# Performance work log

Hardware: AMD Instinct MI355X
Metric: run time of the kernel (lower is better)

## Reference

```python
import jax, jax.numpy as jnp
import numpy as np

DT = 0.01


def setup_inputs() -> dict:
    key = jax.random.key(0)
    ks = jax.random.split(key, 16)
    B, T, IN, S, N, OUT, H = 512, 2048, 32, 16, 128, 8, 64
    sc = 0.1
    return {
        "obs": jax.random.normal(ks[0], (B, T, IN), jnp.float32),
        "x0": jnp.zeros((B, S), jnp.float32),
        "A_T": sc * jax.random.normal(ks[1], (S, S), jnp.float32),
        "Bw_T": sc * jax.random.normal(ks[2], (N, S), jnp.float32),
        "By_T": sc * jax.random.normal(ks[3], (IN, S), jnp.float32),
        "Cv_T": sc * jax.random.normal(ks[4], (S, N), jnp.float32),
        "Dvy_T": sc * jax.random.normal(ks[5], (IN, N), jnp.float32),
        "Cu_T": sc * jax.random.normal(ks[6], (S, OUT), jnp.float32),
        "Duw_T": sc * jax.random.normal(ks[7], (N, OUT), jnp.float32),
        "Duy_T": sc * jax.random.normal(ks[8], (IN, OUT), jnp.float32),
        "log_stds": jnp.full((OUT,), -1.6094379124341003, jnp.float32),
        "W1": sc * jax.random.normal(ks[9], (IN, H), jnp.float32),
        "b1": jnp.zeros((H,), jnp.float32),
        "W2": sc * jax.random.normal(ks[10], (H, H), jnp.float32),
        "b2": jnp.zeros((H,), jnp.float32),
        "W3": sc * jax.random.normal(ks[11], (H, 1), jnp.float32),
        "b3": jnp.zeros((1,), jnp.float32),
    }


def reference(obs, x0, A_T, Bw_T, By_T, Cv_T, Dvy_T, Cu_T, Duw_T, Duy_T,
              log_stds, W1, b1, W2, b2, W3, b3):
    B, T, _ = obs.shape

    def xdot(x, y, w=None):
        if w is None:
            w = jnp.tanh(x @ Cv_T + y @ Dvy_T)
        return x @ A_T + w @ Bw_T + y @ By_T

    def step(x, y):
        # y: [B, IN], x: [B, S]
        w = jnp.tanh(x @ Cv_T + y @ Dvy_T)          # [B, N]
        u = x @ Cu_T + w @ Duw_T + y @ Duy_T        # [B, OUT]
        k1 = xdot(x, y, w=w)
        k2 = xdot(x + DT * k1 / 2, y)
        k3 = xdot(x + DT * k2 / 2, y)
        k4 = xdot(x + DT * k3, y)
        x_next = x + DT / 6 * (k1 + 2 * k2 + 2 * k3 + k4)
        return x_next, u

    obs_t = jnp.swapaxes(obs, 0, 1)                 # [T, B, IN]
    x_final, actions_t = jax.lax.scan(step, x0, obs_t)
    actions = jnp.swapaxes(actions_t, 0, 1)         # [B, T, OUT]

    log_stds_rep = jnp.broadcast_to(log_stds, actions.shape[:2] + log_stds.shape)
    outputs = jnp.concatenate((actions, log_stds_rep), axis=2)

    # value baseline MLP over raw observations
    h = jnp.tanh(obs @ W1 + b1)
    h = jnp.tanh(h @ W2 + b2)
    value = (h @ W3 + b3).reshape(-1)               # [B*T]
    return outputs, x_final, value
```

## Files before the change

### kernel.cpp

```cpp
#include <hip/hip_runtime.h>


#define B_SZ  512
#define T_LEN 2048
#define IN_D  32
#define S_D   16
#define N_D   128
#define OUT_D 8
#define H_D   64
#define DT_C  0.01f

typedef unsigned short u16;
typedef unsigned int   u32;
typedef unsigned int uv2 __attribute__((ext_vector_type(2)));

__device__ __forceinline__ float bf2f(u16 u){ return __uint_as_float(((u32)u)<<16); }
__device__ __forceinline__ float lo2f(u32 w){ return __uint_as_float(w<<16); }
__device__ __forceinline__ float hi2f(u32 w){ return __uint_as_float(w & 0xffff0000u); }
__device__ __forceinline__ u16 f2bf(float f){
    u32 u = __float_as_uint(f);
    u32 r = (u + 0x7fffu + ((u>>16)&1u)) >> 16;
    return (u16)r;
}
__device__ __forceinline__ float fast_tanh(float a){
    float e = __builtin_amdgcn_exp2f(a * 2.8853900817779268f);
    float r = __builtin_amdgcn_rcpf(e + 1.0f);
    return fmaf(-2.0f, r, 1.0f);
}
__device__ __forceinline__ u32 getc(const uint4& v, int c){
    return c==0 ? v.x : c==1 ? v.y : c==2 ? v.z : v.w;
}

#define QUAD1 0xB1
#define QUAD2 0x4E
#define QUAD3 0x1B
#define ROR8  0x128
#define HMIR  0x141
#define RMIR  0x140
template<int CTRL>
__device__ __forceinline__ float dppf(float v){
    return __int_as_float(__builtin_amdgcn_update_dpp(
        __float_as_int(v), __float_as_int(v), CTRL, 0xF, 0xF, false));
}
__device__ __forceinline__ float pl16sum(float v){
    uv2 r = __builtin_amdgcn_permlane16_swap(__float_as_uint(v), __float_as_uint(v), false, false);
    return __uint_as_float(r[0]) + __uint_as_float(r[1]);
}
__device__ __forceinline__ float pl32sum(float v){
    uv2 r = __builtin_amdgcn_permlane32_swap(__float_as_uint(v), __float_as_uint(v), false, false);
    return __uint_as_float(r[0]) + __uint_as_float(r[1]);
}

__device__ __forceinline__ int sig4(int d){ return (d&3) ^ ((d&4)?7:0) ^ (d&8); }
__device__ __forceinline__ int sig3(int d){ return (d&3) ^ ((d&4)?7:0); }

template<bool BF16>
__device__ __forceinline__ float ldw(const void* p, int i){
    if (BF16) return bf2f(((const u16*)p)[i]);
    else      return ((const float*)p)[i];
}
template<bool BF16>
__device__ __forceinline__ float yelem(const uint4* yr, int j){
    if (BF16) { u32 w = getc(yr[j>>3], (j>>1)&3); return (j&1) ? hi2f(w) : lo2f(w); }
    else      { return __uint_as_float(getc(yr[j>>2], j&3)); }
}
template<bool BF16>
__device__ __forceinline__ void ldrow(uint4* r, const void* obs, size_t row){
    const uint4* p = (const uint4*)((const char*)obs + row * (size_t)(IN_D * (BF16 ? 2 : 4)));
    #pragma unroll
    for (int q = 0; q < (BF16 ? 4 : 8); ++q) r[q] = p[q];
}
template<bool BF16>
__device__ __forceinline__ void stout(void* out, size_t i, float v){
    if (BF16) ((u16*)out)[i] = f2bf(v);
    else      ((float*)out)[i] = v;
}

template<bool BF16>
__global__ __launch_bounds__(128, 1)
void rnn_fused(const void* __restrict__ obs,  const void* __restrict__ x0,
               const void* __restrict__ A_T,  const void* __restrict__ Bw_T,
               const void* __restrict__ By_T, const void* __restrict__ Cv_T,
               const void* __restrict__ Dvy_T,const void* __restrict__ Cu_T,
               const void* __restrict__ Duw_T,const void* __restrict__ Duy_T,
               const void* __restrict__ log_stds,
               const void* __restrict__ W1, const void* __restrict__ b1,
               const void* __restrict__ W2, const void* __restrict__ b2,
               const void* __restrict__ W3, const void* __restrict__ b3,
               void* __restrict__ out)
{
    {
        u32 w0 = *(const u32*)log_stds;
        bool is_bf16 = ((w0 & 0xffffu) == 0xBFCEu);
        if (is_bf16 != BF16) return;
    }

    const int b = blockIdx.x;
    const int t = threadIdx.x;
    const int l = t & 63;
    constexpr int NW = BF16 ? 4 : 8;

    __shared__ __align__(16) float yds[2][160];
    __shared__ __align__(16) float vh[2][64];

    const size_t XF_OFF  = (size_t)B_SZ * T_LEN * 16;
    const size_t VAL_OFF = XF_OFF + (size_t)B_SZ * S_D;

    if (t < 64) {
        const int cx = l & 15;
        const int o8 = l & 7;
        const int n0 = l, n1 = l + 64;

        float Cv0x[16], Cv1x[16], AxCol[16], CuCol[16];
        #pragma unroll
        for (int m = 0; m < 16; ++m) {
            int s = cx ^ m;
            Cv0x[m] = ldw<BF16>(Cv_T, s * N_D + n0);
            Cv1x[m] = ldw<BF16>(Cv_T, s * N_D + n1);
            AxCol[m] = ldw<BF16>(A_T,  s * S_D + cx);
            CuCol[m] = ldw<BF16>(Cu_T, s * OUT_D + o8);
        }
        float Bw0x[16], Bw1x[16];
        #pragma unroll
        for (int d = 0; d < 16; ++d) {
            int s = cx ^ sig4(d);
            Bw0x[d] = ldw<BF16>(Bw_T, n0 * S_D + s);
            Bw1x[d] = ldw<BF16>(Bw_T, n1 * S_D + s);
        }
        float Duw0x[8], Duw1x[8];
        #pragma unroll
        for (int d = 0; d < 8; ++d) {
            int o = o8 ^ sig3(d);
            Duw0x[d] = ldw<BF16>(Duw_T, n0 * OUT_D + o);
            Duw1x[d] = ldw<BF16>(Duw_T, n1 * OUT_D + o);
        }
        const float lsv = ldw<BF16>(log_stds, o8);

        float xb = ldw<BF16>(x0, b * S_D + cx);
        float g[16];
        #pragma unroll
        for (int m = 0; m < 16; ++m) g[m] = ldw<BF16>(x0, b * S_D + (cx ^ m));

        __syncthreads();

        for (int step = 0; step < T_LEN; ++step) {
            const float* yb = yds[step & 1];
            float yD0 = yb[l];
            float yD1 = yb[64 + l];
            float yXv = yb[128 + cx];
            float yUv = yb[144 + o8];

            float kacc = 0.f;
            #pragma unroll
            for (int i = 0; i < 4; ++i) {
                float a0a = 0.f, a0b = 0.f, a0c = 0.f, a0d = 0.f;
                float a1a = 0.f, a1b = 0.f, a1c = 0.f, a1d = 0.f;
                #pragma unroll
                for (int m = 0; m < 4; ++m) {
                    a0a = fmaf(g[m],    Cv0x[m],    a0a);
                    a0b = fmaf(g[m+4],  Cv0x[m+4],  a0b);
                    a0c = fmaf(g[m+8],  Cv0x[m+8],  a0c);
                    a0d = fmaf(g[m+12], Cv0x[m+12], a0d);
                    a1a = fmaf(g[m],    Cv1x[m],    a1a);
                    a1b = fmaf(g[m+4],  Cv1x[m+4],  a1b);
                    a1c = fmaf(g[m+8],  Cv1x[m+8],  a1c);
                    a1d = fmaf(g[m+12], Cv1x[m+12], a1d);
                }
                float w0 = fast_tanh(((a0a + a0b) + (a0c + a0d)) + yD0);
                float w1 = fast_tanh(((a1a + a1b) + (a1c + a1d)) + yD1);

                float axAa = 0.f, axAb = 0.f, axAc = 0.f, axAd = 0.f;
                #pragma unroll
                for (int m = 0; m < 4; ++m) {
                    axAa = fmaf(g[m],    AxCol[m],    axAa);
                    axAb = fmaf(g[m+4],  AxCol[m+4],  axAb);
                    axAc = fmaf(g[m+8],  AxCol[m+8],  axAc);
                    axAd = fmaf(g[m+12], AxCol[m+12], axAd);
                }
                float axA = ((axAa + axAb) + (axAc + axAd)) + yXv;

                float pk[16];
                #pragma unroll
                for (int d = 0; d < 16; ++d) pk[d] = fmaf(w1, Bw1x[d], w0 * Bw0x[d]);
                #pragma unroll
                for (int d = 0; d < 16; d += 2) pk[d] += dppf<QUAD1>(pk[d+1]);
                #pragma unroll
                for (int d = 0; d < 16; d += 4) pk[d] += dppf<QUAD2>(pk[d+2]);
                pk[0] += dppf<HMIR>(pk[4]);
                pk[8] += dppf<HMIR>(pk[12]);
                float krow  = pk[0] + dppf<ROR8>(pk[8]);
                float kfull = pl32sum(pl16sum(krow)) + axA;

                if (i == 0) {
                    float axCua = 0.f, axCub = 0.f;
                    #pragma unroll
                    for (int m = 0; m < 8; ++m) {
                        axCua = fmaf(g[m],   CuCol[m],   axCua);
                        axCub = fmaf(g[m+8], CuCol[m+8], axCub);
                    }
                    float pu[8];
                    #pragma unroll
                    for (int d = 0; d < 8; ++d) pu[d] = fmaf(w1, Duw1x[d], w0 * Duw0x[d]);
                    #pragma unroll
                    for (int d = 0; d < 8; d += 2) pu[d] += dppf<QUAD1>(pu[d+1]);
                    pu[0] += dppf<QUAD2>(pu[2]);
                    pu[4] += dppf<QUAD2>(pu[6]);
                    float urow = pu[0] + dppf<HMIR>(pu[4]);
                    urow += dppf<ROR8>(urow);
                    float uo = pl32sum(pl16sum(urow)) + ((axCua + axCub) + yUv);
                    if (l < 16) {
                        size_t ob = ((size_t)b * T_LEN + step) * 16;
                        stout<BF16>(out, ob + l, (l < 8) ? uo : lsv);
                    }
                }

                kacc += ((i == 1 || i == 2) ? 2.0f : 1.0f) * kfull;
                float xnew;
                if (i == 0 || i == 1) xnew = fmaf(0.5f * DT_C, kfull, xb);
                else if (i == 2)      xnew = fmaf(DT_C, kfull, xb);
                else { xb = fmaf(DT_C * (1.0f / 6.0f), kacc, xb); xnew = xb; }

                g[0]  = xnew;
                g[1]  = dppf<QUAD1>(g[0]);
                g[2]  = dppf<QUAD2>(g[0]);
                g[3]  = dppf<QUAD3>(g[0]);
                g[7]  = dppf<HMIR>(g[0]);
                g[6]  = dppf<QUAD1>(g[7]);
                g[5]  = dppf<QUAD2>(g[7]);
                g[4]  = dppf<QUAD3>(g[7]);
                g[8]  = dppf<ROR8>(g[0]);
                g[9]  = dppf<QUAD1>(g[8]);
                g[10] = dppf<QUAD2>(g[8]);
                g[11] = dppf<QUAD3>(g[8]);
                g[15] = dppf<RMIR>(g[0]);
                g[14] = dppf<QUAD1>(g[15]);
                g[13] = dppf<QUAD2>(g[15]);
                g[12] = dppf<QUAD3>(g[15]);
            }
            __syncthreads();
        }
        if (l < 16) {
            stout<BF16>(out, XF_OFF + (size_t)b * S_D + l, xb);
        }
    } else {
        float Dvy0[32], Dvy1[32];
        #pragma unroll
        for (int j = 0; j < 32; ++j) {
            Dvy0[j] = ldw<BF16>(Dvy_T, j * N_D + l);
            Dvy1[j] = ldw<BF16>(Dvy_T, j * N_D + 64 + l);
        }
        float XC[32];
        #pragma unroll
        for (int j = 0; j < 32; ++j) {
            float v = 0.f;
            if (l >= 16 && l < 32) v = ldw<BF16>(By_T,  j * S_D   + (l & 15));
            if (l >= 48 && l < 56) v = ldw<BF16>(Duy_T, j * OUT_D + (l & 7));
            XC[j] = v;
        }
        float W1c[32], W2c[64];
        #pragma unroll
        for (int j = 0; j < 32; ++j) W1c[j] = ldw<BF16>(W1, j * H_D + l);
        #pragma unroll
        for (int j = 0; j < 64; ++j) W2c[j] = ldw<BF16>(W2, j * H_D + l);
        float b1l = ldw<BF16>(b1, l);
        float b2l = ldw<BF16>(b2, l);
        float w3l = ldw<BF16>(W3, l);
        float b3f = ldw<BF16>(b3, 0);

        auto body = [&](int row, const uint4* yc, bool doWork) {
            if (doWork) {
                float d0a=0.f,d0b=0.f,d1a=0.f,d1b=0.f,xea=0.f,xeb=0.f;
                #pragma unroll
                for (int j = 0; j < 16; ++j) {
                    float ya = yelem<BF16>(yc, j), yb2 = yelem<BF16>(yc, j + 16);
                    d0a = fmaf(ya,  Dvy0[j],    d0a);
                    d0b = fmaf(yb2, Dvy0[j+16], d0b);
                    d1a = fmaf(ya,  Dvy1[j],    d1a);
                    d1b = fmaf(yb2, Dvy1[j+16], d1b);
                    xea = fmaf(ya,  XC[j],      xea);
                    xeb = fmaf(yb2, XC[j+16],   xeb);
                }
                float* db = yds[row & 1];
                db[l]      = d0a + d0b;
                db[64 + l] = d1a + d1b;
                float xev = xea + xeb;
                if (l >= 16 && l < 32) db[128 + (l - 16)] = xev;
                if (l >= 48 && l < 56) db[144 + (l - 48)] = xev;

                float h1a = b1l, h1b = 0.f;
                #pragma unroll
                for (int j = 0; j < 16; ++j) {
                    h1a = fmaf(yelem<BF16>(yc, j),      W1c[j],    h1a);
                    h1b = fmaf(yelem<BF16>(yc, j + 16), W1c[j+16], h1b);
                }
                float h1 = fast_tanh(h1a + h1b);
                float* vhb = vh[row & 1];
                vhb[l] = h1;
                float hv[64];
                #pragma unroll
                for (int q = 0; q < 16; ++q) {
                    float4 v4 = *(const float4*)&vhb[q * 4];
                    hv[q*4+0] = v4.x; hv[q*4+1] = v4.y;
                    hv[q*4+2] = v4.z; hv[q*4+3] = v4.w;
                }
                float h2a = b2l, h2b = 0.f, h2c = 0.f, h2d = 0.f;
                #pragma unroll
                for (int j = 0; j < 16; ++j) {
                    h2a = fmaf(hv[j],    W2c[j],    h2a);
                    h2b = fmaf(hv[j+16], W2c[j+16], h2b);
                    h2c = fmaf(hv[j+32], W2c[j+32], h2c);
                    h2d = fmaf(hv[j+48], W2c[j+48], h2d);
                }
                float h2 = fast_tanh((h2a + h2b) + (h2c + h2d));
                float v = h2 * w3l;
                v += dppf<QUAD1>(v);
                v += dppf<QUAD2>(v);
                v += dppf<HMIR>(v);
                v += dppf<ROR8>(v);
                v = pl32sum(pl16sum(v));
                if (l == 0) {
                    size_t r = (size_t)b * T_LEN + row;
                    stout<BF16>(out, VAL_OFF + r, v + b3f);
                }
            }
        };

        uint4 yrA[NW], yrB[NW];
        ldrow<BF16>(yrA, obs, (size_t)b * T_LEN);
        body(0, yrA, true);
        ldrow<BF16>(yrB, obs, (size_t)b * T_LEN + 1);
        __syncthreads();

        for (int s = 0; s < T_LEN; s += 2) {
            {
                int pf = (s + 2 < T_LEN) ? (s + 2) : (T_LEN - 1);
                ldrow<BF16>(yrA, obs, (size_t)b * T_LEN + pf);
                body(s + 1, yrB, true);
                __syncthreads();
            }
            {
                int pf = (s + 3 < T_LEN) ? (s + 3) : (T_LEN - 1);
                ldrow<BF16>(yrB, obs, (size_t)b * T_LEN + pf);
                bool live = (s + 2 < T_LEN);
                body(live ? (s + 2) : 0, yrA, live);
                __syncthreads();
            }
        }
    }
}

extern "C" void kernel_launch(void* const* d_in, const int* in_sizes, int n_in,
                              void* d_out, int out_size, void* d_ws, size_t ws_size,
                              hipStream_t stream) {
    (void)in_sizes; (void)n_in; (void)out_size; (void)d_ws; (void)ws_size;
    rnn_fused<true><<<dim3(B_SZ), dim3(128), 0, stream>>>(
        d_in[0], d_in[1], d_in[2], d_in[3], d_in[4], d_in[5], d_in[6], d_in[7],
        d_in[8], d_in[9], d_in[10], d_in[11], d_in[12], d_in[13], d_in[14],
        d_in[15], d_in[16], d_out);
    rnn_fused<false><<<dim3(B_SZ), dim3(128), 0, stream>>>(
        d_in[0], d_in[1], d_in[2], d_in[3], d_in[4], d_in[5], d_in[6], d_in[7],
        d_in[8], d_in[9], d_in[10], d_in[11], d_in[12], d_in[13], d_in[14],
        d_in[15], d_in[16], d_out);
}
```

Baseline: 2.990 ms.

## Batch producer/consumer handoff into 8-step chunks to cut per-step barriers

The shared-memory staging buffer for precomputed input projections grows from one step per slot to an 8-step chunk per slot, still double-buffered. The producer wave now computes a whole chunk of rows ahead, and both waves synchronise once per chunk instead of once per timestep. This takes block barriers off the serial RK4 recurrence path, at the cost of more LDS and a longer pipeline fill. The launch bounds are also re-expressed with a waves-per-EU attribute, and the value-MLP inner loop is lightly restructured.

```diff
diff --git a/kernel.cpp b/kernel.cpp
--- a/kernel.cpp
+++ b/kernel.cpp
@@ -9,6 +9,8 @@
 #define OUT_D 8
 #define H_D   64
 #define DT_C  0.01f
+#define CHUNK 8
+#define NCH   (T_LEN / CHUNK)
 
 typedef unsigned short u16;
 typedef unsigned int   u32;
@@ -77,7 +79,7 @@
 }
 
 template<bool BF16>
-__global__ __launch_bounds__(128, 1)
+__global__ __attribute__((amdgpu_waves_per_eu(1, 1))) __launch_bounds__(128)
 void rnn_fused(const void* __restrict__ obs,  const void* __restrict__ x0,
                const void* __restrict__ A_T,  const void* __restrict__ Bw_T,
                const void* __restrict__ By_T, const void* __restrict__ Cv_T,
@@ -100,7 +102,7 @@
     const int l = t & 63;
     constexpr int NW = BF16 ? 4 : 8;
 
-    __shared__ __align__(16) float yds[2][160];
+    __shared__ __align__(16) float yds[2][CHUNK][160];
     __shared__ __align__(16) float vh[2][64];
 
     const size_t XF_OFF  = (size_t)B_SZ * T_LEN * 16;
@@ -143,99 +145,110 @@
 
         __syncthreads();
 
-        for (int step = 0; step < T_LEN; ++step) {
-            const float* yb = yds[step & 1];
-            float yD0 = yb[l];
-            float yD1 = yb[64 + l];
-            float yXv = yb[128 + cx];
-            float yUv = yb[144 + o8];
-
-            float kacc = 0.f;
-            #pragma unroll
-            for (int i = 0; i < 4; ++i) {
-                float a0a = 0.f, a0b = 0.f, a0c = 0.f, a0d = 0.f;
-                float a1a = 0.f, a1b = 0.f, a1c = 0.f, a1d = 0.f;
+        for (int r = 0; r < NCH; ++r) {
+            const float (*yb)[160] = yds[r & 1];
+            float nD0 = yb[0][l];
+            float nD1 = yb[0][64 + l];
+            float nXv = yb[0][128 + cx];
+            float nUv = yb[0][144 + o8];
+
+            for (int j = 0; j < CHUNK; ++j) {
+                const float yD0 = nD0, yD1 = nD1, yXv = nXv, yUv = nUv;
+                if (j + 1 < CHUNK) {
+                    nD0 = yb[j+1][l];
+                    nD1 = yb[j+1][64 + l];
+                    nXv = yb[j+1][128 + cx];
+                    nUv = yb[j+1][144 + o8];
+                }
+                const int step = r * CHUNK + j;
+
+                float kacc = 0.f;
                 #pragma unroll
-                for (int m = 0; m < 4; ++m) {
-                    a0a = fmaf(g[m],    Cv0x[m],    a0a);
-                    a0b = fmaf(g[m+4],  Cv0x[m+4],  a0b);
-                    a0c = fmaf(g[m+8],  Cv0x[m+8],  a0c);
-                    a0d = fmaf(g[m+12], Cv0x[m+12], a0d);
-                    a1a = fmaf(g[m],    Cv1x[m],    a1a);
-                    a1b = fmaf(g[m+4],  Cv1x[m+4],  a1b);
-                    a1c = fmaf(g[m+8],  Cv1x[m+8],  a1c);
-                    a1d = fmaf(g[m+12], Cv1x[m+12], a1d);
+                for (int i = 0; i < 4; ++i) {
+                    float a0a = 0.f, a0b = 0.f, a0c = 0.f, a0d = 0.f;
+                    float a1a = 0.f, a1b = 0.f, a1c = 0.f, a1d = 0.f;
+                    #pragma unroll
+                    for (int m = 0; m < 4; ++m) {
+                        a0a = fmaf(g[m],    Cv0x[m],    a0a);
+                        a0b = fmaf(g[m+4],  Cv0x[m+4],  a0b);
+                        a0c = fmaf(g[m+8],  Cv0x[m+8],  a0c);
+                        a0d = fmaf(g[m+12], Cv0x[m+12], a0d);
+                        a1a = fmaf(g[m],    Cv1x[m],    a1a);
+                        a1b = fmaf(g[m+4],  Cv1x[m+4],  a1b);
+                        a1c = fmaf(g[m+8],  Cv1x[m+8],  a1c);
+                        a1d = fmaf(g[m+12], Cv1x[m+12], a1d);
+                    }
+                    float w0 = fast_tanh(((a0a + a0b) + (a0c + a0d)) + yD0);
+                    float w1 = fast_tanh(((a1a + a1b) + (a1c + a1d)) + yD1);
+
+                    float axAa = 0.f, axAb = 0.f, axAc = 0.f, axAd = 0.f;
+                    #pragma unroll
+                    for (int m = 0; m < 4; ++m) {
+                        axAa = fmaf(g[m],    AxCol[m],    axAa);
+                        axAb = fmaf(g[m+4],  AxCol[m+4],  axAb);
+                        axAc = fmaf(g[m+8],  AxCol[m+8],  axAc);
+                        axAd = fmaf(g[m+12], AxCol[m+12], axAd);
+                    }
+                    float axA = ((axAa + axAb) + (axAc + axAd)) + yXv;
+
+                    float pk[16];
+                    #pragma unroll
+                    for (int d = 0; d < 16; ++d) pk[d] = fmaf(w1, Bw1x[d], w0 * Bw0x[d]);
+                    #pragma unroll
+                    for (int d = 0; d < 16; d += 2) pk[d] += dppf<QUAD1>(pk[d+1]);
+                    #pragma unroll
+                    for (int d = 0; d < 16; d += 4) pk[d] += dppf<QUAD2>(pk[d+2]);
+                    pk[0] += dppf<HMIR>(pk[4]);
+                    pk[8] += dppf<HMIR>(pk[12]);
+                    float krow  = pk[0] + dppf<ROR8>(pk[8]);
+                    float kfull = pl32sum(pl16sum(krow)) + axA;
+
+                    if (i == 0) {
+                        float axCua = 0.f, axCub = 0.f;
+                        #pragma unroll
+                        for (int m = 0; m < 8; ++m) {
+                            axCua = fmaf(g[m],   CuCol[m],   axCua);
+                            axCub = fmaf(g[m+8], CuCol[m+8], axCub);
+                        }
+                        float pu[8];
+                        #pragma unroll
+                        for (int d = 0; d < 8; ++d) pu[d] = fmaf(w1, Duw1x[d], w0 * Duw0x[d]);
+                        #pragma unroll
+                        for (int d = 0; d < 8; d += 2) pu[d] += dppf<QUAD1>(pu[d+1]);
+                        pu[0] += dppf<QUAD2>(pu[2]);
+                        pu[4] += dppf<QUAD2>(pu[6]);
+                        float urow = pu[0] + dppf<HMIR>(pu[4]);
+                        urow += dppf<ROR8>(urow);
+                        float uo = pl32sum(pl16sum(urow)) + ((axCua + axCub) + yUv);
+                        if (l < 16) {
+                            size_t ob = ((size_t)b * T_LEN + step) * 16;
+                            stout<BF16>(out, ob + l, (l < 8) ? uo : lsv);
+                        }
+                    }
+
+                    kacc += ((i == 1 || i == 2) ? 2.0f : 1.0f) * kfull;
+                    float xnew;
+                    if (i == 0 || i == 1) xnew = fmaf(0.5f * DT_C, kfull, xb);
+                    else if (i == 2)      xnew = fmaf(DT_C, kfull, xb);
+                    else { xb = fmaf(DT_C * (1.0f / 6.0f), kacc, xb); xnew = xb; }
+
+                    g[0]  = xnew;
+                    g[1]  = dppf<QUAD1>(g[0]);
+                    g[2]  = dppf<QUAD2>(g[0]);
+                    g[3]  = dppf<QUAD3>(g[0]);
+                    g[7]  = dppf<HMIR>(g[0]);
+                    g[6]  = dppf<QUAD1>(g[7]);
+                    g[5]  = dppf<QUAD2>(g[7]);
+                    g[4]  = dppf<QUAD3>(g[7]);
+                    g[8]  = dppf<ROR8>(g[0]);
+                    g[9]  = dppf<QUAD1>(g[8]);
+                    g[10] = dppf<QUAD2>(g[8]);
+                    g[11] = dppf<QUAD3>(g[8]);
+                    g[15] = dppf<RMIR>(g[0]);
+                    g[14] = dppf<QUAD1>(g[15]);
+                    g[13] = dppf<QUAD2>(g[15]);
+                    g[12] = dppf<QUAD3>(g[15]);
                 }
-                float w0 = fast_tanh(((a0a + a0b) + (a0c + a0d)) + yD0);
-                float w1 = fast_tanh(((a1a + a1b) + (a1c + a1d)) + yD1);
-
-                float axAa = 0.f, axAb = 0.f, axAc = 0.f, axAd = 0.f;
-                #pragma unroll
-                for (int m = 0; m < 4; ++m) {
-                    axAa = fmaf(g[m],    AxCol[m],    axAa);
-                    axAb = fmaf(g[m+4],  AxCol[m+4],  axAb);
-                    axAc = fmaf(g[m+8],  AxCol[m+8],  axAc);
-                    axAd = fmaf(g[m+12], AxCol[m+12], axAd);
-                }
-                float axA = ((axAa + axAb) + (axAc + axAd)) + yXv;
-
-                float pk[16];
-                #pragma unroll
-                for (int d = 0; d < 16; ++d) pk[d] = fmaf(w1, Bw1x[d], w0 * Bw0x[d]);
-                #pragma unroll
-                for (int d = 0; d < 16; d += 2) pk[d] += dppf<QUAD1>(pk[d+1]);
-                #pragma unroll
-                for (int d = 0; d < 16; d += 4) pk[d] += dppf<QUAD2>(pk[d+2]);
-                pk[0] += dppf<HMIR>(pk[4]);
-                pk[8] += dppf<HMIR>(pk[12]);
-                float krow  = pk[0] + dppf<ROR8>(pk[8]);
-                float kfull = pl32sum(pl16sum(krow)) + axA;
-
-                if (i == 0) {
-                    float axCua = 0.f, axCub = 0.f;
-                    #pragma unroll
-                    for (int m = 0; m < 8; ++m) {
-                        axCua = fmaf(g[m],   CuCol[m],   axCua);
-                        axCub = fmaf(g[m+8], CuCol[m+8], axCub);
-                    }
-                    float pu[8];
-                    #pragma unroll
-                    for (int d = 0; d < 8; ++d) pu[d] = fmaf(w1, Duw1x[d], w0 * Duw0x[d]);
-                    #pragma unroll
-                    for (int d = 0; d < 8; d += 2) pu[d] += dppf<QUAD1>(pu[d+1]);
-                    pu[0] += dppf<QUAD2>(pu[2]);
-                    pu[4] += dppf<QUAD2>(pu[6]);
-                    float urow = pu[0] + dppf<HMIR>(pu[4]);
-                    urow += dppf<ROR8>(urow);
-                    float uo = pl32sum(pl16sum(urow)) + ((axCua + axCub) + yUv);
-                    if (l < 16) {
-                        size_t ob = ((size_t)b * T_LEN + step) * 16;
-                        stout<BF16>(out, ob + l, (l < 8) ? uo : lsv);
-                    }
-                }
-
-                kacc += ((i == 1 || i == 2) ? 2.0f : 1.0f) * kfull;
-                float xnew;
-                if (i == 0 || i == 1) xnew = fmaf(0.5f * DT_C, kfull, xb);
-                else if (i == 2)      xnew = fmaf(DT_C, kfull, xb);
-                else { xb = fmaf(DT_C * (1.0f / 6.0f), kacc, xb); xnew = xb; }
-
-                g[0]  = xnew;
-                g[1]  = dppf<QUAD1>(g[0]);
-                g[2]  = dppf<QUAD2>(g[0]);
-                g[3]  = dppf<QUAD3>(g[0]);
-                g[7]  = dppf<HMIR>(g[0]);
-                g[6]  = dppf<QUAD1>(g[7]);
-                g[5]  = dppf<QUAD2>(g[7]);
-                g[4]  = dppf<QUAD3>(g[7]);
-                g[8]  = dppf<ROR8>(g[0]);
-                g[9]  = dppf<QUAD1>(g[8]);
-                g[10] = dppf<QUAD2>(g[8]);
-                g[11] = dppf<QUAD3>(g[8]);
-                g[15] = dppf<RMIR>(g[0]);
-                g[14] = dppf<QUAD1>(g[15]);
-                g[13] = dppf<QUAD2>(g[15]);
-                g[12] = dppf<QUAD3>(g[15]);
             }
             __syncthreads();
         }
@@ -267,84 +280,81 @@
         float w3l = ldw<BF16>(W3, l);
         float b3f = ldw<BF16>(b3, 0);
 
-        auto body = [&](int row, const uint4* yc, bool doWork) {
-            if (doWork) {
-                float d0a=0.f,d0b=0.f,d1a=0.f,d1b=0.f,xea=0.f,xeb=0.f;
-                #pragma unroll
-                for (int j = 0; j < 16; ++j) {
-                    float ya = yelem<BF16>(yc, j), yb2 = yelem<BF16>(yc, j + 16);
-                    d0a = fmaf(ya,  Dvy0[j],    d0a);
-                    d0b = fmaf(yb2, Dvy0[j+16], d0b);
-                    d1a = fmaf(ya,  Dvy1[j],    d1a);
-                    d1b = fmaf(yb2, Dvy1[j+16], d1b);
-                    xea = fmaf(ya,  XC[j],      xea);
-                    xeb = fmaf(yb2, XC[j+16],   xeb);
-                }
-                float* db = yds[row & 1];
-                db[l]      = d0a + d0b;
-                db[64 + l] = d1a + d1b;
-                float xev = xea + xeb;
-                if (l >= 16 && l < 32) db[128 + (l - 16)] = xev;
-                if (l >= 48 && l < 56) db[144 + (l - 48)] = xev;
-
-                float h1a = b1l, h1b = 0.f;
-                #pragma unroll
-                for (int j = 0; j < 16; ++j) {
-                    h1a = fmaf(yelem<BF16>(yc, j),      W1c[j],    h1a);
-                    h1b = fmaf(yelem<BF16>(yc, j + 16), W1c[j+16], h1b);
-                }
-                float h1 = fast_tanh(h1a + h1b);
-                float* vhb = vh[row & 1];
-                vhb[l] = h1;
-                float hv[64];
-                #pragma unroll
-                for (int q = 0; q < 16; ++q) {
-                    float4 v4 = *(const float4*)&vhb[q * 4];
-                    hv[q*4+0] = v4.x; hv[q*4+1] = v4.y;
-                    hv[q*4+2] = v4.z; hv[q*4+3] = v4.w;
-                }
-                float h2a = b2l, h2b = 0.f, h2c = 0.f, h2d = 0.f;
-                #pragma unroll
-                for (int j = 0; j < 16; ++j) {
-                    h2a = fmaf(hv[j],    W2c[j],    h2a);
-                    h2b = fmaf(hv[j+16], W2c[j+16], h2b);
-                    h2c = fmaf(hv[j+32], W2c[j+32], h2c);
-                    h2d = fmaf(hv[j+48], W2c[j+48], h2d);
-                }
-                float h2 = fast_tanh((h2a + h2b) + (h2c + h2d));
-                float v = h2 * w3l;
-                v += dppf<QUAD1>(v);
-                v += dppf<QUAD2>(v);
-                v += dppf<HMIR>(v);
-                v += dppf<ROR8>(v);
-                v = pl32sum(pl16sum(v));
-                if (l == 0) {
-                    size_t r = (size_t)b * T_LEN + row;
-                    stout<BF16>(out, VAL_OFF + r, v + b3f);
-                }
+        auto body = [&](int row, const uint4* yc) {
+            float d0a=0.f,d0b=0.f,d1a=0.f,d1b=0.f,xea=0.f,xeb=0.f;
+            #pragma unroll
+            for (int j = 0; j < 16; ++j) {
+                float ya = yelem<BF16>(yc, j), yb2 = yelem<BF16>(yc, j + 16);
+                d0a = fmaf(ya,  Dvy0[j],    d0a);
+                d0b = fmaf(yb2, Dvy0[j+16], d0b);
+                d1a = fmaf(ya,  Dvy1[j],    d1a);
+                d1b = fmaf(yb2, Dvy1[j+16], d1b);
+                xea = fmaf(ya,  XC[j],      xea);
+                xeb = fmaf(yb2, XC[j+16],   xeb);
+            }
+            float* db = yds[(row / CHUNK) & 1][row % CHUNK];
+            db[l]      = d0a + d0b;
+            db[64 + l] = d1a + d1b;
+            float xev = xea + xeb;
+            if (l >= 16 && l < 32) db[128 + (l - 16)] = xev;
+            if (l >= 48 && l < 56) db[144 + (l - 48)] = xev;
+
+            float h1a = b1l, h1b = 0.f;
+            #pragma unroll
+            for (int j = 0; j < 16; ++j) {
+                h1a = fmaf(yelem<BF16>(yc, j),      W1c[j],    h1a);
+                h1b = fmaf(yelem<BF16>(yc, j + 16), W1c[j+16], h1b);
+            }
+            float h1 = fast_tanh(h1a + h1b);
+            float* vhb = vh[row & 1];
+            vhb[l] = h1;
+            float h2a = b2l, h2b = 0.f, h2c = 0.f, h2d = 0.f;
+            #pragma unroll
+            for (int q = 0; q < 16; ++q) {
+                float4 v4 = *(const float4*)&vhb[q * 4];
+                float* acc = (q & 2) ? ((q & 1) ? &h2d : &h2c)
+                                     : ((q & 1) ? &h2b : &h2a);
+                *acc = fmaf(v4.x, W2c[q*4+0], *acc);
+                *acc = fmaf(v4.y, W2c[q*4+1], *acc);
+                *acc = fmaf(v4.z, W2c[q*4+2], *acc);
+                *acc = fmaf(v4.w, W2c[q*4+3], *acc);
+            }
+            float h2 = fast_tanh((h2a + h2b) + (h2c + h2d));
+            float v = h2 * w3l;
+            v += dppf<QUAD1>(v);
+            v += dppf<QUAD2>(v);
+            v += dppf<HMIR>(v);
+            v += dppf<ROR8>(v);
+            v = pl32sum(pl16sum(v));
+            if (l == 0) {
+                size_t rr = (size_t)b * T_LEN + row;
+                stout<BF16>(out, VAL_OFF + rr, v + b3f);
             }
         };
 
         uint4 yrA[NW], yrB[NW];
-        ldrow<BF16>(yrA, obs, (size_t)b * T_LEN);
-        body(0, yrA, true);
-        ldrow<BF16>(yrB, obs, (size_t)b * T_LEN + 1);
+        const size_t base = (size_t)b * T_LEN;
+        ldrow<BF16>(yrA, obs, base + 0);
+        ldrow<BF16>(yrB, obs, base + 1);
+
+        auto produce = [&](int c) {
+            for (int jj = 0; jj < CHUNK; jj += 2) {
+                int row = c * CHUNK + jj;
+                body(row, yrA);
+                { int nr = row + 2; if (nr > T_LEN - 1) nr = T_LEN - 1;
+                  ldrow<BF16>(yrA, obs, base + nr); }
+                body(row + 1, yrB);
+                { int nr = row + 3; if (nr > T_LEN - 1) nr = T_LEN - 1;
+                  ldrow<BF16>(yrB, obs, base + nr); }
+            }
+        };
+
+        produce(0);
         __syncthreads();
 
-        for (int s = 0; s < T_LEN; s += 2) {
-            {
-                int pf = (s + 2 < T_LEN) ? (s + 2) : (T_LEN - 1);
-                ldrow<BF16>(yrA, obs, (size_t)b * T_LEN + pf);
-                body(s + 1, yrB, true);
-                __syncthreads();
-            }
-            {
-                int pf = (s + 3 < T_LEN) ? (s + 3) : (T_LEN - 1);
-                ldrow<BF16>(yrB, obs, (size_t)b * T_LEN + pf);
-                bool live = (s + 2 < T_LEN);
-                body(live ? (s + 2) : 0, yrA, live);
-                __syncthreads();
-            }
+        for (int r = 0; r < NCH; ++r) {
+            if (r < NCH - 1) produce(r + 1);
+            __syncthreads();
         }
     }
 }
```

Result: no change. 3.022 ms (+1.1%).
